# Performance work log

Hardware: AMD Instinct MI355X
Metric: run time of the kernel (lower is better)

## Reference

```python
import jax, jax.numpy as jnp
import numpy as np

B, C_IN, H, W = 16, 16, 256, 256  # B must equal out_channels for the module's broadcast
C_OUT = 16


def setup_inputs() -> dict:
    key = jax.random.key(0)
    k1, k2, k3, k4 = jax.random.split(key, 4)
    return {
        "x_real": jax.random.normal(k1, (B, C_IN, H, W), dtype=jnp.float32),
        "x_imag": jax.random.normal(k2, (B, C_IN, H, W), dtype=jnp.float32),
        "w_real": jax.random.normal(k3, (C_OUT, C_IN, H, W), dtype=jnp.float32),
        "w_imag": jax.random.normal(k4, (C_OUT, C_IN, H, W), dtype=jnp.float32),
    }


def reference(x_real, x_imag, w_real, w_imag):
    # HolographicConv: ifft2(fft2(x) * W).real with complex x and W.
    x = jax.lax.complex(x_real, x_imag)            # (B, C_in, H, W) complex64
    w = jax.lax.complex(w_real, w_imag)            # (C_out, C_in, H, W) complex64
    x_freq = jnp.fft.fft2(x, axes=(-2, -1))
    conv_freq = x_freq * w                          # broadcast: B == C_out, k == H == W
    out = jnp.fft.ifft2(conv_freq, axes=(-2, -1))
    return out.real.astype(jnp.float32)
```

## Files before the change

kernel.cpp:

```cpp
#include <hip/hip_runtime.h>


#define PI_F 3.14159265358979323846f

__device__ __forceinline__ float2 cadd(float2 a, float2 b){ return make_float2(a.x+b.x, a.y+b.y); }
__device__ __forceinline__ float2 csub(float2 a, float2 b){ return make_float2(a.x-b.x, a.y-b.y); }
__device__ __forceinline__ float2 cmul(float2 a, float2 b){
  return make_float2(a.x*b.x - a.y*b.y, a.x*b.y + a.y*b.x);
}

__device__ __forceinline__ int SW(int e){ return e ^ (e >> 4); }

template<int DIR>
__device__ __forceinline__ void bfly4(float2& a, float2& b, float2& c, float2& d,
                                      float2 w1, float2 w2, float2 w3)
{
  float2 apc = cadd(a,c), amc = csub(a,c);
  float2 bpd = cadd(b,d), bmd = csub(b,d);
  float2 jb = (DIR > 0) ? make_float2(-bmd.y, bmd.x)
                        : make_float2( bmd.y,-bmd.x);
  a = cadd(apc, bpd);
  b = cmul(w1, csub(amc, jb));
  c = cmul(w2, csub(apc, bpd));
  d = cmul(w3, cadd(amc, jb));
}

template<int DIR>
__device__ __forceinline__ void fft256_x2(float2 va[4], float2 vb[4],
                                          float2* sa, float2* sb,
                                          const float2* tw, int lane)
{
  #pragma unroll
  for (int st = 0; st < 3; ++st) {
    const int s  = 1 << (2*st);
    const int ps = lane & ~(s-1);
    const int q  = lane &  (s-1);
    float2 w1 = tw[ps];
    float2 w2 = tw[(2*ps) & 255];
    float2 w3 = tw[(3*ps) & 255];
    if (DIR < 0) { w1.y = -w1.y; w2.y = -w2.y; w3.y = -w3.y; }
    bfly4<DIR>(va[0], va[1], va[2], va[3], w1, w2, w3);
    bfly4<DIR>(vb[0], vb[1], vb[2], vb[3], w1, w2, w3);
    const int dbase = q + 4*ps;
    __builtin_amdgcn_wave_barrier();
    sa[SW(dbase + 0*s)] = va[0];
    sb[SW(dbase + 0*s)] = vb[0];
    sa[SW(dbase + 1*s)] = va[1];
    sb[SW(dbase + 1*s)] = vb[1];
    sa[SW(dbase + 2*s)] = va[2];
    sb[SW(dbase + 2*s)] = vb[2];
    sa[SW(dbase + 3*s)] = va[3];
    sb[SW(dbase + 3*s)] = vb[3];
    __builtin_amdgcn_wave_barrier();
    va[0] = sa[SW(lane +   0)];
    vb[0] = sb[SW(lane +   0)];
    va[1] = sa[SW(lane +  64)];
    vb[1] = sb[SW(lane +  64)];
    va[2] = sa[SW(lane + 128)];
    vb[2] = sb[SW(lane + 128)];
    va[3] = sa[SW(lane + 192)];
    vb[3] = sb[SW(lane + 192)];
    __builtin_amdgcn_wave_barrier();
  }
  const float2 one = make_float2(1.f, 0.f);
  bfly4<DIR>(va[0], va[1], va[2], va[3], one, one, one);
  bfly4<DIR>(vb[0], vb[1], vb[2], vb[3], one, one, one);
}

__device__ __forceinline__ void init_tw(float2* tw, int tid)
{
  float sv, cv;
  sincosf(-2.0f * PI_F * (float)tid / 256.0f, &sv, &cv);
  tw[tid] = make_float2(cv, sv);
}

__global__ __launch_bounds__(256, 3) void k_colfft(const float* __restrict__ xr,
                                                   const float* __restrict__ xi,
                                                   float2* __restrict__ wsT)
{
  __shared__ float2 xt[256][17];
  __shared__ float2 scr[4][2][256];
  __shared__ float2 tw[256];
  const int tid = threadIdx.x;
  init_tw(tw, tid);
  const int imgl = blockIdx.x >> 4;
  const int v0   = (blockIdx.x & 15) * 16;
  const size_t ib = (size_t)imgl * 65536;
  const int c  = tid & 15;
  const int h0 = tid >> 4;
  #pragma unroll
  for (int t = 0; t < 16; ++t) {
    const int u = t*16 + h0;
    xt[u][c] = make_float2(xr[ib + (size_t)u*256 + v0 + c],
                           xi[ib + (size_t)u*256 + v0 + c]);
  }
  __syncthreads();
  const int wave = tid >> 6, lane = tid & 63;
  #pragma unroll 1
  for (int cc = 0; cc < 2; ++cc) {
    const int colA = wave*4 + cc*2, colB = colA + 1;
    float2 va[4], vb[4];
    #pragma unroll
    for (int r = 0; r < 4; ++r) { va[r] = xt[lane + 64*r][colA];
                                  vb[r] = xt[lane + 64*r][colB]; }
    fft256_x2<1>(va, vb, scr[wave][0], scr[wave][1], tw, lane);
    float2* oA = wsT + ib + (size_t)(v0 + colA)*256;
    float2* oB = wsT + ib + (size_t)(v0 + colB)*256;
    #pragma unroll
    for (int r = 0; r < 4; ++r) { oA[lane + 64*r] = va[r];
                                  oB[lane + 64*r] = vb[r]; }
  }
}

__global__ __launch_bounds__(256, 3) void k_rowpass(float2* __restrict__ wsT,
                                                    const float* __restrict__ wr,
                                                    const float* __restrict__ wi,
                                                    int img0)
{
  __shared__ float2 xt[256][17];
  __shared__ float2 scr[4][2][256];
  __shared__ float2 tw[256];
  const int tid = threadIdx.x;
  init_tw(tw, tid);
  const int imgl = blockIdx.x >> 4;
  const int k0   = (blockIdx.x & 15) * 16;
  const size_t ib = (size_t)imgl * 65536;
  const size_t wb = (size_t)(img0 + imgl) * 65536;
  const int c  = tid & 15;
  const int h0 = tid >> 4;
  #pragma unroll
  for (int t = 0; t < 16; ++t) {
    const int v = t*16 + h0;
    xt[v][c] = wsT[ib + (size_t)v*256 + k0 + c];
  }
  __syncthreads();
  const int wave = tid >> 6, lane = tid & 63;
  #pragma unroll 1
  for (int cc = 0; cc < 2; ++cc) {
    const int colA = wave*4 + cc*2, colB = colA + 1;
    float2 va[4], vb[4];
    #pragma unroll
    for (int r = 0; r < 4; ++r) { va[r] = xt[lane + 64*r][colA];
                                  vb[r] = xt[lane + 64*r][colB]; }
    fft256_x2<1>(va, vb, scr[wave][0], scr[wave][1], tw, lane);
    const float* wrA = wr + wb + (size_t)(k0 + colA)*256;
    const float* wiA = wi + wb + (size_t)(k0 + colA)*256;
    const float* wrB = wr + wb + (size_t)(k0 + colB)*256;
    const float* wiB = wi + wb + (size_t)(k0 + colB)*256;
    #pragma unroll
    for (int r = 0; r < 4; ++r) {
      const int l = lane + 64*r;
      va[r] = cmul(va[r], make_float2(wrA[l], wiA[l]));
      vb[r] = cmul(vb[r], make_float2(wrB[l], wiB[l]));
    }
    fft256_x2<-1>(va, vb, scr[wave][0], scr[wave][1], tw, lane);
    #pragma unroll
    for (int r = 0; r < 4; ++r) { xt[lane + 64*r][colA] = va[r];
                                  xt[lane + 64*r][colB] = vb[r]; }
  }
  __syncthreads();
  #pragma unroll
  for (int t = 0; t < 16; ++t) {
    const int v = t*16 + h0;
    wsT[ib + (size_t)v*256 + k0 + c] = xt[v][c];
  }
}

__global__ __launch_bounds__(256, 3) void k_rowifft(const float2* __restrict__ wsT,
                                                    float* __restrict__ out)
{
  __shared__ float ot[256][17];
  __shared__ float2 scr[4][2][256];
  __shared__ float2 tw[256];
  const int tid = threadIdx.x;
  init_tw(tw, tid);
  __syncthreads();
  const int imgl = blockIdx.x >> 4;
  const int v0   = (blockIdx.x & 15) * 16;
  const size_t ib = (size_t)imgl * 65536;
  const int wave = tid >> 6, lane = tid & 63;
  const float sc = 1.0f / 65536.0f;
  #pragma unroll 1
  for (int cc = 0; cc < 2; ++cc) {
    const int colA = wave*4 + cc*2, colB = colA + 1;
    const float2* pA = wsT + ib + (size_t)(v0 + colA)*256;
    const float2* pB = wsT + ib + (size_t)(v0 + colB)*256;
    float2 va[4], vb[4];
    #pragma unroll
    for (int r = 0; r < 4; ++r) { va[r] = pA[lane + 64*r];
                                  vb[r] = pB[lane + 64*r]; }
    fft256_x2<-1>(va, vb, scr[wave][0], scr[wave][1], tw, lane);
    #pragma unroll
    for (int r = 0; r < 4; ++r) { ot[lane + 64*r][colA] = va[r].x * sc;
                                  ot[lane + 64*r][colB] = vb[r].x * sc; }
  }
  __syncthreads();
  const int c  = tid & 15;
  const int h0 = tid >> 4;
  #pragma unroll
  for (int t = 0; t < 16; ++t) {
    const int u = t*16 + h0;
    out[ib + (size_t)u*256 + v0 + c] = ot[u][c];
  }
}

extern "C" void kernel_launch(void* const* d_in, const int* in_sizes, int n_in,
                              void* d_out, int out_size, void* d_ws, size_t ws_size,
                              hipStream_t stream)
{
  const float* xr = (const float*)d_in[0];
  const float* xi = (const float*)d_in[1];
  const float* wr = (const float*)d_in[2];
  const float* wi = (const float*)d_in[3];
  float* out = (float*)d_out;

  const int IMG = 256;
  const size_t per_img = (size_t)65536 * sizeof(float2);
  int ipc = (int)(ws_size / per_img);
  if (ipc < 1)   ipc = 1;
  if (ipc > IMG) ipc = IMG;
  float2* wsp = (float2*)d_ws;

  for (int img0 = 0; img0 < IMG; img0 += ipc) {
    const int n = (IMG - img0 < ipc) ? (IMG - img0) : ipc;
    k_colfft <<<dim3(n*16), dim3(256), 0, stream>>>(xr + (size_t)img0*65536,
                                                    xi + (size_t)img0*65536, wsp);
    k_rowpass<<<dim3(n*16), dim3(256), 0, stream>>>(wsp, wr, wi, img0);
    k_rowifft<<<dim3(n*16), dim3(256), 0, stream>>>(wsp, out + (size_t)img0*65536);
  }
}
```

Measured before the change: 180.6 us.

## Process four FFT columns per wave and alias transpose tile with scratch LDS

Each wave now runs its four 256-point column FFTs together instead of two passes of two. The transpose tile and FFT scratch share one LDS pool, which cuts shared memory per block so occupancy can rise from 3 to 4 blocks per CU. In the row pass, the W weight loads are issued before the forward FFT so their latency overlaps compute. The risk is higher register pressure from holding 16 or 32 complex values per thread under a tighter launch bound, which could cause spills.

```diff
diff --git a/kernel.cpp b/kernel.cpp
--- a/kernel.cpp
+++ b/kernel.cpp
@@ -26,8 +26,7 @@
 }
 
 template<int DIR>
-__device__ __forceinline__ void fft256_x2(float2 va[4], float2 vb[4],
-                                          float2* sa, float2* sb,
+__device__ __forceinline__ void fft256_x4(float2 v[4][4], float2* scr,
                                           const float2* tw, int lane)
 {
   #pragma unroll
@@ -39,32 +38,34 @@
     float2 w2 = tw[(2*ps) & 255];
     float2 w3 = tw[(3*ps) & 255];
     if (DIR < 0) { w1.y = -w1.y; w2.y = -w2.y; w3.y = -w3.y; }
-    bfly4<DIR>(va[0], va[1], va[2], va[3], w1, w2, w3);
-    bfly4<DIR>(vb[0], vb[1], vb[2], vb[3], w1, w2, w3);
+    #pragma unroll
+    for (int c = 0; c < 4; ++c)
+      bfly4<DIR>(v[c][0], v[c][1], v[c][2], v[c][3], w1, w2, w3);
     const int dbase = q + 4*ps;
     __builtin_amdgcn_wave_barrier();
-    sa[SW(dbase + 0*s)] = va[0];
-    sb[SW(dbase + 0*s)] = vb[0];
-    sa[SW(dbase + 1*s)] = va[1];
-    sb[SW(dbase + 1*s)] = vb[1];
-    sa[SW(dbase + 2*s)] = va[2];
-    sb[SW(dbase + 2*s)] = vb[2];
-    sa[SW(dbase + 3*s)] = va[3];
-    sb[SW(dbase + 3*s)] = vb[3];
+    #pragma unroll
+    for (int c = 0; c < 4; ++c) {
+      float2* s_ = scr + c*256;
+      s_[SW(dbase + 0*s)] = v[c][0];
+      s_[SW(dbase + 1*s)] = v[c][1];
+      s_[SW(dbase + 2*s)] = v[c][2];
+      s_[SW(dbase + 3*s)] = v[c][3];
+    }
     __builtin_amdgcn_wave_barrier();
-    va[0] = sa[SW(lane +   0)];
-    vb[0] = sb[SW(lane +   0)];
-    va[1] = sa[SW(lane +  64)];
-    vb[1] = sb[SW(lane +  64)];
-    va[2] = sa[SW(lane + 128)];
-    vb[2] = sb[SW(lane + 128)];
-    va[3] = sa[SW(lane + 192)];
-    vb[3] = sb[SW(lane + 192)];
+    #pragma unroll
+    for (int c = 0; c < 4; ++c) {
+      float2* s_ = scr + c*256;
+      v[c][0] = s_[SW(lane +   0)];
+      v[c][1] = s_[SW(lane +  64)];
+      v[c][2] = s_[SW(lane + 128)];
+      v[c][3] = s_[SW(lane + 192)];
+    }
     __builtin_amdgcn_wave_barrier();
   }
   const float2 one = make_float2(1.f, 0.f);
-  bfly4<DIR>(va[0], va[1], va[2], va[3], one, one, one);
-  bfly4<DIR>(vb[0], vb[1], vb[2], vb[3], one, one, one);
+  #pragma unroll
+  for (int c = 0; c < 4; ++c)
+    bfly4<DIR>(v[c][0], v[c][1], v[c][2], v[c][3], one, one, one);
 }
 
 __device__ __forceinline__ void init_tw(float2* tw, int tid)
@@ -74,12 +75,11 @@
   tw[tid] = make_float2(cv, sv);
 }
 
-__global__ __launch_bounds__(256, 3) void k_colfft(const float* __restrict__ xr,
+__global__ __launch_bounds__(256, 4) void k_colfft(const float* __restrict__ xr,
                                                    const float* __restrict__ xi,
                                                    float2* __restrict__ wsT)
 {
-  __shared__ float2 xt[256][17];
-  __shared__ float2 scr[4][2][256];
+  __shared__ float2 pool[4352];
   __shared__ float2 tw[256];
   const int tid = threadIdx.x;
   init_tw(tw, tid);
@@ -91,34 +91,33 @@
   #pragma unroll
   for (int t = 0; t < 16; ++t) {
     const int u = t*16 + h0;
-    xt[u][c] = make_float2(xr[ib + (size_t)u*256 + v0 + c],
-                           xi[ib + (size_t)u*256 + v0 + c]);
+    pool[u*17 + c] = make_float2(xr[ib + (size_t)u*256 + v0 + c],
+                                 xi[ib + (size_t)u*256 + v0 + c]);
   }
   __syncthreads();
   const int wave = tid >> 6, lane = tid & 63;
-  #pragma unroll 1
-  for (int cc = 0; cc < 2; ++cc) {
-    const int colA = wave*4 + cc*2, colB = colA + 1;
-    float2 va[4], vb[4];
-    #pragma unroll
-    for (int r = 0; r < 4; ++r) { va[r] = xt[lane + 64*r][colA];
-                                  vb[r] = xt[lane + 64*r][colB]; }
-    fft256_x2<1>(va, vb, scr[wave][0], scr[wave][1], tw, lane);
-    float2* oA = wsT + ib + (size_t)(v0 + colA)*256;
-    float2* oB = wsT + ib + (size_t)(v0 + colB)*256;
-    #pragma unroll
-    for (int r = 0; r < 4; ++r) { oA[lane + 64*r] = va[r];
-                                  oB[lane + 64*r] = vb[r]; }
-  }
-}
-
-__global__ __launch_bounds__(256, 3) void k_rowpass(float2* __restrict__ wsT,
+  float2 v[4][4];
+  #pragma unroll
+  for (int cq = 0; cq < 4; ++cq)
+    #pragma unroll
+    for (int r = 0; r < 4; ++r)
+      v[cq][r] = pool[(lane + 64*r)*17 + wave*4 + cq];
+  __syncthreads();
+  fft256_x4<1>(v, pool + wave*1024, tw, lane);
+  #pragma unroll
+  for (int cq = 0; cq < 4; ++cq) {
+    float2* o = wsT + ib + (size_t)(v0 + wave*4 + cq)*256;
+    #pragma unroll
+    for (int r = 0; r < 4; ++r) o[lane + 64*r] = v[cq][r];
+  }
+}
+
+__global__ __launch_bounds__(256, 4) void k_rowpass(float2* __restrict__ wsT,
                                                     const float* __restrict__ wr,
                                                     const float* __restrict__ wi,
                                                     int img0)
 {
-  __shared__ float2 xt[256][17];
-  __shared__ float2 scr[4][2][256];
+  __shared__ float2 pool[4352];
   __shared__ float2 tw[256];
   const int tid = threadIdx.x;
   init_tw(tw, tid);
@@ -130,77 +129,84 @@
   const int h0 = tid >> 4;
   #pragma unroll
   for (int t = 0; t < 16; ++t) {
-    const int v = t*16 + h0;
-    xt[v][c] = wsT[ib + (size_t)v*256 + k0 + c];
+    const int vv = t*16 + h0;
+    pool[vv*17 + c] = wsT[ib + (size_t)vv*256 + k0 + c];
   }
   __syncthreads();
   const int wave = tid >> 6, lane = tid & 63;
-  #pragma unroll 1
-  for (int cc = 0; cc < 2; ++cc) {
-    const int colA = wave*4 + cc*2, colB = colA + 1;
-    float2 va[4], vb[4];
-    #pragma unroll
-    for (int r = 0; r < 4; ++r) { va[r] = xt[lane + 64*r][colA];
-                                  vb[r] = xt[lane + 64*r][colB]; }
-    fft256_x2<1>(va, vb, scr[wave][0], scr[wave][1], tw, lane);
-    const float* wrA = wr + wb + (size_t)(k0 + colA)*256;
-    const float* wiA = wi + wb + (size_t)(k0 + colA)*256;
-    const float* wrB = wr + wb + (size_t)(k0 + colB)*256;
-    const float* wiB = wi + wb + (size_t)(k0 + colB)*256;
+  float2 v[4][4];
+  #pragma unroll
+  for (int cq = 0; cq < 4; ++cq)
+    #pragma unroll
+    for (int r = 0; r < 4; ++r)
+      v[cq][r] = pool[(lane + 64*r)*17 + wave*4 + cq];
+  __syncthreads();
+  float2 wv[4][4];
+  #pragma unroll
+  for (int cq = 0; cq < 4; ++cq) {
+    const size_t base = wb + (size_t)(k0 + wave*4 + cq)*256;
     #pragma unroll
     for (int r = 0; r < 4; ++r) {
       const int l = lane + 64*r;
-      va[r] = cmul(va[r], make_float2(wrA[l], wiA[l]));
-      vb[r] = cmul(vb[r], make_float2(wrB[l], wiB[l]));
+      wv[cq][r] = make_float2(wr[base + l], wi[base + l]);
     }
-    fft256_x2<-1>(va, vb, scr[wave][0], scr[wave][1], tw, lane);
-    #pragma unroll
-    for (int r = 0; r < 4; ++r) { xt[lane + 64*r][colA] = va[r];
-                                  xt[lane + 64*r][colB] = vb[r]; }
-  }
-  __syncthreads();
-  #pragma unroll
-  for (int t = 0; t < 16; ++t) {
-    const int v = t*16 + h0;
-    wsT[ib + (size_t)v*256 + k0 + c] = xt[v][c];
-  }
-}
-
-__global__ __launch_bounds__(256, 3) void k_rowifft(const float2* __restrict__ wsT,
+  }
+  fft256_x4<1>(v, pool + wave*1024, tw, lane);
+  #pragma unroll
+  for (int cq = 0; cq < 4; ++cq)
+    #pragma unroll
+    for (int r = 0; r < 4; ++r)
+      v[cq][r] = cmul(v[cq][r], wv[cq][r]);
+  fft256_x4<-1>(v, pool + wave*1024, tw, lane);
+  __syncthreads();
+  #pragma unroll
+  for (int cq = 0; cq < 4; ++cq)
+    #pragma unroll
+    for (int r = 0; r < 4; ++r)
+      pool[(lane + 64*r)*17 + wave*4 + cq] = v[cq][r];
+  __syncthreads();
+  #pragma unroll
+  for (int t = 0; t < 16; ++t) {
+    const int vv = t*16 + h0;
+    wsT[ib + (size_t)vv*256 + k0 + c] = pool[vv*17 + c];
+  }
+}
+
+__global__ __launch_bounds__(256, 4) void k_rowifft(const float2* __restrict__ wsT,
                                                     float* __restrict__ out)
 {
-  __shared__ float ot[256][17];
-  __shared__ float2 scr[4][2][256];
+  __shared__ float2 pool[4096];
   __shared__ float2 tw[256];
   const int tid = threadIdx.x;
   init_tw(tw, tid);
-  __syncthreads();
   const int imgl = blockIdx.x >> 4;
   const int v0   = (blockIdx.x & 15) * 16;
   const size_t ib = (size_t)imgl * 65536;
   const int wave = tid >> 6, lane = tid & 63;
+  float2 v[4][4];
+  #pragma unroll
+  for (int cq = 0; cq < 4; ++cq) {
+    const float2* p = wsT + ib + (size_t)(v0 + wave*4 + cq)*256;
+    #pragma unroll
+    for (int r = 0; r < 4; ++r) v[cq][r] = p[lane + 64*r];
+  }
+  __syncthreads();
+  fft256_x4<-1>(v, pool + wave*1024, tw, lane);
+  __syncthreads();
+  float* ot = (float*)pool;
   const float sc = 1.0f / 65536.0f;
-  #pragma unroll 1
-  for (int cc = 0; cc < 2; ++cc) {
-    const int colA = wave*4 + cc*2, colB = colA + 1;
-    const float2* pA = wsT + ib + (size_t)(v0 + colA)*256;
-    const float2* pB = wsT + ib + (size_t)(v0 + colB)*256;
-    float2 va[4], vb[4];
-    #pragma unroll
-    for (int r = 0; r < 4; ++r) { va[r] = pA[lane + 64*r];
-                                  vb[r] = pB[lane + 64*r]; }
-    fft256_x2<-1>(va, vb, scr[wave][0], scr[wave][1], tw, lane);
-    #pragma unroll
-    for (int r = 0; r < 4; ++r) { ot[lane + 64*r][colA] = va[r].x * sc;
-                                  ot[lane + 64*r][colB] = vb[r].x * sc; }
-  }
+  #pragma unroll
+  for (int cq = 0; cq < 4; ++cq)
+    #pragma unroll
+    for (int r = 0; r < 4; ++r)
+      ot[(lane + 64*r)*17 + wave*4 + cq] = v[cq][r].x * sc;
   __syncthreads();
   const int c  = tid & 15;
   const int h0 = tid >> 4;
   #pragma unroll
   for (int t = 0; t < 16; ++t) {
     const int u = t*16 + h0;
-    out[ib + (size_t)u*256 + v0 + c] = ot[u][c];
+    out[ib + (size_t)u*256 + v0 + c] = ot[u*17 + c];
   }
 }
 
```

New measurement: 224.6 us. 24.4% more time.
